# Kernel tuning notes

Hardware: AMD Instinct MI355X
Metric: run time of the kernel (lower is better)

The kernel has to match this reference:

```python
import jax, jax.numpy as jnp
import numpy as np

CONF_THRES = 0.4
IOU_THRES = 0.45
MAX_WH = 4096.0   # class offset for non-agnostic NMS (torch code: max_wh)
K_PRE = 1024      # candidates kept for the O(K^2) NMS stage (<= max_nms=30000)
MAX_DET = 300     # max detections per image (torch default)
B, N, NC = 16, 25200, 80


def xywh2xyxy(x):
    xy, wh = x[..., :2], x[..., 2:4]
    return jnp.concatenate([xy - wh * 0.5, xy + wh * 0.5], axis=-1)


def box_iou(a, b):
    # a: [K,4], b: [K,4] in xyxy
    area_a = (a[:, 2] - a[:, 0]) * (a[:, 3] - a[:, 1])
    area_b = (b[:, 2] - b[:, 0]) * (b[:, 3] - b[:, 1])
    lt = jnp.maximum(a[:, None, :2], b[None, :, :2])
    rb = jnp.minimum(a[:, None, 2:], b[None, :, 2:])
    inter = jnp.clip(rb - lt, 0.0, None).prod(-1)
    return inter / (area_a[:, None] + area_b[None, :] - inter + 1e-7)


def _nms_single(pred, conf_logit, logit, head):
    # pred [N,85] (decoded, sigmoided), conf_logit [N,5] raw, logit [N,80] raw, head [N]
    xc = pred[:, 4] > CONF_THRES                      # objectness gate
    obj_sig = jax.nn.sigmoid(conf_logit[:, 4:5])      # [N,1]
    log_sig = jax.nn.sigmoid(logit) * obj_sig         # sel_prob == 'objclass'
    cls_scores = pred[:, 5:] * pred[:, 4:5]           # x[:,5:] *= x[:,4:5]
    box = xywh2xyxy(pred[:, :4])                      # [N,4]
    conf = cls_scores.max(axis=1)                     # best class conf
    j = cls_scores.argmax(axis=1).astype(pred.dtype)  # best class id
    valid = xc & (conf > CONF_THRES)
    score = jnp.where(valid, conf, 0.0)
    # top-K candidates (sorted descending) -> fixed-shape NMS
    top_s, top_i = jax.lax.top_k(score, K_PRE)
    valid_k = top_s > 0.0
    boxes_k = box[top_i] + j[top_i, None] * MAX_WH    # per-class box offset (agnostic=False)
    iou = box_iou(boxes_k, boxes_k)                   # [K,K]
    idx = jnp.arange(K_PRE)

    def body(i, keep):
        sup = (iou[i] > IOU_THRES) & (idx > i) & keep[i]
        return keep & ~sup

    keep = jax.lax.fori_loop(0, K_PRE, body, valid_k)
    final_score = jnp.where(keep, top_s, 0.0)
    _, sel = jax.lax.top_k(final_score, MAX_DET)      # first MAX_DET survivors
    gi = top_i[sel]
    m = (final_score[sel] > 0.0).astype(pred.dtype)[:, None]  # validity mask
    det = jnp.concatenate([box[gi], conf[gi, None], j[gi, None]], axis=1)  # [300,6] xyxy,conf,cls
    # pack: det(6) | class logits*obj(80) | obj_conf(1) | classHead(1) | valid(1) -> [300,89]
    return jnp.concatenate(
        [det * m, log_sig[gi] * m, obj_sig[gi] * m, head[gi, None] * m, m], axis=1)


def setup_inputs() -> dict:
    key = jax.random.key(0)
    k1, k2, k3, k4, k5, k6 = jax.random.split(key, 6)
    xy = jax.random.uniform(k1, (B, N, 2), jnp.float32) * 640.0
    wh = 2.0 + jax.random.uniform(k2, (B, N, 2), jnp.float32) * 198.0
    objcls = jax.random.uniform(k3, (B, N, 1 + NC), jnp.float32)
    prediction = jnp.concatenate([xy, wh, objcls], axis=-1)       # [B,N,85]
    pred_conf_logits = jax.random.normal(k4, (B, N, 5), jnp.float32)
    logits = jax.random.normal(k5, (B, N, NC), jnp.float32)
    class_head = jax.random.randint(k6, (B, N), 0, 3).astype(jnp.float32)
    return {"prediction": prediction, "pred_conf_logits": pred_conf_logits,
            "logits": logits, "class_head": class_head}


def reference(prediction, pred_conf_logits, logits, class_head):
    return jax.vmap(_nms_single)(prediction, pred_conf_logits, logits, class_head)
```

## Files before the change

kernel.cpp:

```cpp
#include <hip/hip_runtime.h>
#include <math.h>

#define BATCH 16
#define NN 25200
#define NCLS 80
#define K_PRE 1024
#define MAX_DET 300
#define CONF_T 0.4f
#define IOU_T 0.45f
#define TBIAS 0x3E000000u
#define RROWS 128
#define STHREADS 512

__global__ void __launch_bounds__(STHREADS) score_kernel(
    const float* __restrict__ pred, unsigned long long* __restrict__ keys) {
    __shared__ float srow[RROWS * 85];

    const int tile = blockIdx.x, b = blockIdx.y, tid = threadIdx.x;
    const int row0 = tile * RROWS;
    int nrows = NN - row0;
    if (nrows > RROWS) nrows = RROWS;

    const float4* g4 = (const float4*)(pred + ((size_t)b * NN + row0) * 85);
    float4* l4 = (float4*)srow;
    const int nf4 = (nrows * 85) >> 2;
    for (int i = tid; i < nf4; i += STHREADS) l4[i] = g4[i];
    __syncthreads();

    const int r = tid >> 2, sub = tid & 3;
    float best = 0.0f;
    int bc = sub * 20;
    float obj = 0.0f;
    if (r < nrows) {
        obj = srow[r * 85 + 4];
        if (obj > CONF_T) {
            const float* cp = &srow[r * 85 + 5 + sub * 20];
#pragma unroll
            for (int i = 0; i < 20; ++i) {
                float v = cp[i] * obj;
                if (v > best) { best = v; bc = sub * 20 + i; }
            }
        }
    }
#pragma unroll
    for (int d = 1; d < 4; d <<= 1) {
        float ov = __shfl_xor(best, d);
        int oc = __shfl_xor(bc, d);
        if (ov > best || (ov == best && oc < bc)) { best = ov; bc = oc; }
    }
    if (r < nrows && sub == 0) {
        unsigned t = (obj > CONF_T && best > CONF_T)
                         ? (__float_as_uint(best) - TBIAS) : 0u;
        int n = row0 + r;
        keys[(size_t)b * NN + n] =
            ((unsigned long long)t << 22) |
            ((unsigned long long)(unsigned)(NN - 1 - n) << 7) | (unsigned)bc;
    }
}

__global__ void __launch_bounds__(1024) fused_kernel(
    const unsigned long long* __restrict__ keys,
    const float* __restrict__ pred,
    const float* __restrict__ conf_logits,
    const float* __restrict__ logits,
    const float* __restrict__ head,
    float* __restrict__ out) {
    __shared__ unsigned sA[1024], sB[1024];
    __shared__ unsigned long long skeys[2048];
    __shared__ float bx0[K_PRE], by0[K_PRE], bx1[K_PRE], by1[K_PRE],
        bar_[K_PRE], bsc[K_PRE];
    __shared__ unsigned char bcls[K_PRE];
    __shared__ unsigned short bgi[K_PRE];
    __shared__ unsigned char bkeep[K_PRE];
    __shared__ unsigned sel_d0, sel_cnt;

    const int b = blockIdx.x, tid = threadIdx.x;
    const unsigned long long* bk = keys + (size_t)b * NN;

    sA[tid] = 0u;
    __syncthreads();
    for (int base = 0; base < 25600; base += 1024) {
        int i = base + tid;
        if (i < NN) {
            unsigned t = (unsigned)(bk[i] >> 22);
            if (t) atomicAdd(&sA[t >> 15], 1u);
        }
    }
    __syncthreads();

    unsigned* src = sA;
    unsigned* dst = sB;
    for (int off = 1; off < 1024; off <<= 1) {
        dst[tid] = src[tid] + ((tid + off < 1024) ? src[tid + off] : 0u);
        __syncthreads();
        unsigned* t2 = src; src = dst; dst = t2;
    }
    unsigned total = src[0];
    unsigned K = total < 1024u ? total : 1024u;
    if (tid == 0) { sel_d0 = 0u; sel_cnt = 0u; }
    skeys[tid] = 0ull;
    skeys[tid + 1024] = 0ull;
    __syncthreads();
    if (total) {
        unsigned geq = src[tid];
        unsigned gt = (tid < 1023) ? src[tid + 1] : 0u;
        if (gt < K && K <= geq) sel_d0 = (unsigned)tid;
    }
    __syncthreads();
    const unsigned d0 = sel_d0;

    for (int base = 0; base < 25600; base += 1024) {
        int i = base + tid;
        if (i < NN) {
            unsigned long long key = bk[i];
            unsigned t = (unsigned)(key >> 22);
            if (t && (t >> 15) >= d0) {
                unsigned p = atomicAdd(&sel_cnt, 1u);
                if (p < 2048u) skeys[p] = key;
            }
        }
    }
    __syncthreads();

    for (unsigned k2 = 2; k2 <= 2048; k2 <<= 1) {
        for (unsigned j = k2 >> 1; j > 0; j >>= 1) {
            unsigned i = ((tid & ~(j - 1)) << 1) | (tid & (j - 1));
            unsigned ixj = i | j;
            unsigned long long a = skeys[i], c = skeys[ixj];
            bool desc = ((i & k2) == 0u);
            if (desc ? (a < c) : (a > c)) { skeys[i] = c; skeys[ixj] = a; }
            __syncthreads();
        }
    }

    {
        unsigned long long key = skeys[tid];
        unsigned t = (unsigned)(key >> 22);
        int n = NN - 1 - (int)((key >> 7) & 32767u);
        bkeep[tid] = 0;
        bgi[tid] = (unsigned short)n;
        if (t == 0u) {
            bcls[tid] = 255;
            bsc[tid] = 0.0f;
        } else {
            const float* row = pred + ((size_t)b * NN + n) * 85;
            float x = row[0], y = row[1], w = row[2], h = row[3];
            float vx0 = x - w * 0.5f, vy0 = y - h * 0.5f;
            float vx1 = x + w * 0.5f, vy1 = y + h * 0.5f;
            bx0[tid] = vx0; by0[tid] = vy0; bx1[tid] = vx1; by1[tid] = vy1;
            bar_[tid] = (vx1 - vx0) * (vy1 - vy0);
            bsc[tid] = __uint_as_float(t + TBIAS);
            bcls[tid] = (unsigned char)(key & 127u);
        }
    }
    __syncthreads();

    {
        const int lane = tid & 63;
        const int wv = tid >> 6;
        unsigned char myc[16];
#pragma unroll
        for (int k = 0; k < 16; ++k) myc[k] = bcls[(k << 6) | lane];

        for (int ci = 0; ci < 5; ++ci) {
            const int c = wv + (ci << 4);
            unsigned alive = 0u;
#pragma unroll
            for (int k = 0; k < 16; ++k)
                if (myc[k] == (unsigned char)c) alive |= (1u << k);
            unsigned keptm = 0u;
            for (;;) {
                int s = alive ? ((__builtin_ctz(alive) << 6) | lane)
                              : (1 << 30);
#pragma unroll
                for (int d = 32; d; d >>= 1) {
                    int o = __shfl_xor(s, d);
                    s = o < s ? o : s;
                }
                if (s >= (1 << 30)) break;
                if ((s & 63) == lane) {
                    alive &= ~(1u << (s >> 6));
                    keptm |= (1u << (s >> 6));
                }
                float ax0 = bx0[s], ay0 = by0[s], ax1 = bx1[s], ay1 = by1[s];
                float aa = bar_[s];
                unsigned rem = alive;
                while (rem) {
                    int k = __builtin_ctz(rem);
                    rem &= rem - 1;
                    int j = (k << 6) | lane;
                    float lx = fmaxf(ax0, bx0[j]);
                    float ly = fmaxf(ay0, by0[j]);
                    float rx = fminf(ax1, bx1[j]);
                    float ry = fminf(ay1, by1[j]);
                    float iw = fmaxf(rx - lx, 0.0f);
                    float ih = fmaxf(ry - ly, 0.0f);
                    float inter = iw * ih;
                    float iou = inter / (aa + bar_[j] - inter + 1e-7f);
                    if (iou > IOU_T) alive &= ~(1u << k);
                }
            }
            while (keptm) {
                int k = __builtin_ctz(keptm);
                keptm &= keptm - 1;
                bkeep[(k << 6) | lane] = 1;
            }
        }
    }
    __syncthreads();

    int kp = (int)bkeep[tid];
    src = sA; dst = sB;
    src[tid] = (unsigned)kp;
    __syncthreads();
    for (int off = 1; off < 1024; off <<= 1) {
        dst[tid] = src[tid] + ((tid >= off) ? src[tid - off] : 0u);
        __syncthreads();
        unsigned* t2 = src; src = dst; dst = t2;
    }
    int rank = (int)src[tid] - kp;
    int kcnt = (int)src[1023];

    if (kp && rank < MAX_DET) {
        int gi = (int)bgi[tid];
        float* orow = out + ((size_t)b * MAX_DET + rank) * 89;
        orow[0] = bx0[tid]; orow[1] = by0[tid];
        orow[2] = bx1[tid]; orow[3] = by1[tid];
        orow[4] = bsc[tid];
        orow[5] = (float)bcls[tid];
        float cl = conf_logits[((size_t)b * NN + gi) * 5 + 4];
        float obj_sig = 1.0f / (1.0f + expf(-cl));
        const float4* lrow4 =
            (const float4*)(logits + ((size_t)b * NN + gi) * NCLS);
#pragma unroll 4
        for (int q = 0; q < 20; ++q) {
            float4 l4 = lrow4[q];
            orow[6 + 4 * q + 0] = obj_sig / (1.0f + expf(-l4.x));
            orow[6 + 4 * q + 1] = obj_sig / (1.0f + expf(-l4.y));
            orow[6 + 4 * q + 2] = obj_sig / (1.0f + expf(-l4.z));
            orow[6 + 4 * q + 3] = obj_sig / (1.0f + expf(-l4.w));
        }
        orow[86] = obj_sig;
        orow[87] = head[(size_t)b * NN + gi];
        orow[88] = 1.0f;
    }
    if (tid < MAX_DET && tid >= kcnt) {
        float* orow = out + ((size_t)b * MAX_DET + tid) * 89;
#pragma unroll
        for (int q = 0; q < 89; ++q) orow[q] = 0.0f;
    }
}

extern "C" void kernel_launch(void* const* d_in, const int* in_sizes, int n_in,
                              void* d_out, int out_size, void* d_ws,
                              size_t ws_size, hipStream_t stream) {
    const float* pred        = (const float*)d_in[0];
    const float* conf_logits = (const float*)d_in[1];
    const float* logits      = (const float*)d_in[2];
    const float* head        = (const float*)d_in[3];
    float* out = (float*)d_out;

    unsigned long long* keys = (unsigned long long*)d_ws;

    dim3 sgrid((NN + RROWS - 1) / RROWS, BATCH);
    score_kernel<<<sgrid, STHREADS, 0, stream>>>(pred, keys);
    fused_kernel<<<BATCH, 1024, 0, stream>>>(keys, pred, conf_logits, logits,
                                             head, out);
}
```

Measured before the change: 359.6 us.

## Replace bitonic sort with bucketed scatter and in-bucket rank counting

The top-K selection no longer runs a full 2048-element bitonic sort in shared memory. Keys are now cached in registers so global memory is read only once. The histogram's suffix sums give each score bucket a base offset, keys are scattered into their buckets, and each key's final rank comes from counting larger keys within its own bucket. This removes many barrier-separated sort passes, but adds register pressure (25 64-bit keys per thread) and a serial in-bucket scan whose cost grows with bucket size.

```diff
diff --git a/kernel.cpp b/kernel.cpp
--- a/kernel.cpp
+++ b/kernel.cpp
@@ -11,6 +11,7 @@
 #define TBIAS 0x3E000000u
 #define RROWS 128
 #define STHREADS 512
+#define KITER 25
 
 __global__ void __launch_bounds__(STHREADS) score_kernel(
     const float* __restrict__ pred, unsigned long long* __restrict__ keys) {
@@ -66,25 +67,33 @@
     const float* __restrict__ head,
     float* __restrict__ out) {
     __shared__ unsigned sA[1024], sB[1024];
-    __shared__ unsigned long long skeys[2048];
+    __shared__ unsigned sBC[1024];
+    __shared__ unsigned long long sKeys[2048];
     __shared__ float bx0[K_PRE], by0[K_PRE], bx1[K_PRE], by1[K_PRE],
         bar_[K_PRE], bsc[K_PRE];
     __shared__ unsigned char bcls[K_PRE];
     __shared__ unsigned short bgi[K_PRE];
     __shared__ unsigned char bkeep[K_PRE];
-    __shared__ unsigned sel_d0, sel_cnt;
 
     const int b = blockIdx.x, tid = threadIdx.x;
     const unsigned long long* bk = keys + (size_t)b * NN;
 
+    unsigned long long kreg[KITER];
+#pragma unroll
+    for (int k = 0; k < KITER; ++k) {
+        int i = (k << 10) + tid;
+        kreg[k] = (i < NN) ? bk[i] : 0ull;
+    }
+
     sA[tid] = 0u;
-    __syncthreads();
-    for (int base = 0; base < 25600; base += 1024) {
-        int i = base + tid;
-        if (i < NN) {
-            unsigned t = (unsigned)(bk[i] >> 22);
-            if (t) atomicAdd(&sA[t >> 15], 1u);
-        }
+    sBC[tid] = 0u;
+    sKeys[tid] = 0ull;
+    sKeys[tid + 1024] = 0ull;
+    __syncthreads();
+#pragma unroll
+    for (int k = 0; k < KITER; ++k) {
+        unsigned t = (unsigned)(kreg[k] >> 22);
+        if (t) atomicAdd(&sA[t >> 15], 1u);
     }
     __syncthreads();
 
@@ -95,62 +104,51 @@
         __syncthreads();
         unsigned* t2 = src; src = dst; dst = t2;
     }
-    unsigned total = src[0];
-    unsigned K = total < 1024u ? total : 1024u;
-    if (tid == 0) { sel_d0 = 0u; sel_cnt = 0u; }
-    skeys[tid] = 0ull;
-    skeys[tid + 1024] = 0ull;
-    __syncthreads();
-    if (total) {
-        unsigned geq = src[tid];
-        unsigned gt = (tid < 1023) ? src[tid + 1] : 0u;
-        if (gt < K && K <= geq) sel_d0 = (unsigned)tid;
-    }
-    __syncthreads();
-    const unsigned d0 = sel_d0;
-
-    for (int base = 0; base < 25600; base += 1024) {
-        int i = base + tid;
-        if (i < NN) {
-            unsigned long long key = bk[i];
+    const unsigned* S = src;
+
+#pragma unroll
+    for (int k = 0; k < KITER; ++k) {
+        unsigned long long key = kreg[k];
+        unsigned t = (unsigned)(key >> 22);
+        if (t) {
+            unsigned d = t >> 15;
+            unsigned base = (d < 1023u) ? S[d + 1] : 0u;
+            if (base < 1024u) {
+                unsigned pos = base + atomicAdd(&sBC[d], 1u);
+                if (pos < 2048u) sKeys[pos] = key;
+            }
+        }
+    }
+    bcls[tid] = 255;
+    bsc[tid] = 0.0f;
+    bkeep[tid] = 0;
+    __syncthreads();
+
+#pragma unroll
+    for (int half = 0; half < 2; ++half) {
+        int i = tid + (half << 10);
+        unsigned long long key = sKeys[i];
+        if (key) {
             unsigned t = (unsigned)(key >> 22);
-            if (t && (t >> 15) >= d0) {
-                unsigned p = atomicAdd(&sel_cnt, 1u);
-                if (p < 2048u) skeys[p] = key;
-            }
-        }
-    }
-    __syncthreads();
-
-    for (unsigned k2 = 2; k2 <= 2048; k2 <<= 1) {
-        for (unsigned j = k2 >> 1; j > 0; j >>= 1) {
-            unsigned i = ((tid & ~(j - 1)) << 1) | (tid & (j - 1));
-            unsigned ixj = i | j;
-            unsigned long long a = skeys[i], c = skeys[ixj];
-            bool desc = ((i & k2) == 0u);
-            if (desc ? (a < c) : (a > c)) { skeys[i] = c; skeys[ixj] = a; }
-            __syncthreads();
-        }
-    }
-
-    {
-        unsigned long long key = skeys[tid];
-        unsigned t = (unsigned)(key >> 22);
-        int n = NN - 1 - (int)((key >> 7) & 32767u);
-        bkeep[tid] = 0;
-        bgi[tid] = (unsigned short)n;
-        if (t == 0u) {
-            bcls[tid] = 255;
-            bsc[tid] = 0.0f;
-        } else {
-            const float* row = pred + ((size_t)b * NN + n) * 85;
-            float x = row[0], y = row[1], w = row[2], h = row[3];
-            float vx0 = x - w * 0.5f, vy0 = y - h * 0.5f;
-            float vx1 = x + w * 0.5f, vy1 = y + h * 0.5f;
-            bx0[tid] = vx0; by0[tid] = vy0; bx1[tid] = vx1; by1[tid] = vy1;
-            bar_[tid] = (vx1 - vx0) * (vy1 - vy0);
-            bsc[tid] = __uint_as_float(t + TBIAS);
-            bcls[tid] = (unsigned char)(key & 127u);
+            unsigned d = t >> 15;
+            unsigned seg = (d < 1023u) ? S[d + 1] : 0u;
+            unsigned end = seg + sBC[d];
+            if (end > 2048u) end = 2048u;
+            unsigned r = seg;
+            for (unsigned j = seg; j < end; ++j)
+                if (sKeys[j] > key) ++r;
+            if (r < 1024u) {
+                int n = NN - 1 - (int)((key >> 7) & 32767u);
+                const float* row = pred + ((size_t)b * NN + n) * 85;
+                float x = row[0], y = row[1], w = row[2], h = row[3];
+                float vx0 = x - w * 0.5f, vy0 = y - h * 0.5f;
+                float vx1 = x + w * 0.5f, vy1 = y + h * 0.5f;
+                bx0[r] = vx0; by0[r] = vy0; bx1[r] = vx1; by1[r] = vy1;
+                bar_[r] = (vx1 - vx0) * (vy1 - vy0);
+                bsc[r] = __uint_as_float(t + TBIAS);
+                bcls[r] = (unsigned char)(key & 127u);
+                bgi[r] = (unsigned short)n;
+            }
         }
     }
     __syncthreads();
```

Result: faster. 346.1 us (-3.8%).
